# Kernel optimization log

Hardware: AMD Instinct MI355X
Metric: run time of the kernel (lower is better)

Reference implementation:

```python
import jax, jax.numpy as jnp
import numpy as np

B, L, S, H, E = 4, 1024, 1024, 16, 64
TOP_K = 10


def setup_inputs() -> dict:
    key = jax.random.key(0)
    kq, kk, kv = jax.random.split(key, 3)
    queries = jax.random.normal(kq, (B, L, H, E), dtype=jnp.float32)
    keys = jax.random.normal(kk, (B, S, H, E), dtype=jnp.float32)
    values = jax.random.normal(kv, (B, S, H, E), dtype=jnp.float32)
    return {"queries": queries, "keys": keys, "values": values}


def reference(queries, keys, values):
    Bq, Lq, Hq, Eq = queries.shape
    Sq = keys.shape[1]
    scale = 1.0 / np.sqrt(Eq).astype(np.float32)

    # FFT-based top-k frequency selection (mirrors torch: rfft over seq dim, ortho norm)
    keys_flat = keys.transpose(0, 2, 1, 3).reshape(Bq * Hq, Sq, Eq)  # [BH, S, E]
    freqs = jnp.fft.rfft(keys_flat, axis=1, norm='ortho')            # [BH, S//2+1, E]
    freq_mags = jnp.abs(freqs).mean(axis=-1)                          # [BH, S//2+1]
    k = min(TOP_K, Sq, freq_mags.shape[1])
    _, top_idx = jax.lax.top_k(freq_mags, k)                          # [BH, k]

    # Vectorized scatter of top-k indices into boolean position mask [BH, S]
    sparse_mask = jnp.zeros((Bq * Hq, Sq), dtype=bool)
    sparse_mask = sparse_mask.at[jnp.arange(Bq * Hq)[:, None], top_idx].set(True)
    sparse_mask = sparse_mask.reshape(Bq, Hq, Sq)                     # [B, H, S]

    # Dense masked attention
    scores = jnp.einsum('blhe,bshe->bhls', queries, keys) * scale     # [B, H, L, S]
    scores = jnp.where(sparse_mask[:, :, None, :], scores, -jnp.inf)
    attn = jax.nn.softmax(scores, axis=-1)                            # dropout: eval mode (identity)
    out = jnp.einsum('bhls,bshe->blhe', attn, values)                 # [B, L, H, E]
    return out, attn
```

## Files before the change

### kernel.cpp

```cpp
#include <hip/hip_runtime.h>
#include <math.h>

#define Bc 4
#define Lc 1024
#define Sc 1024
#define Hc 16
#define Ec 64
#define BHc 64
#define NF 513
#define TOPK 10
#define NCH 8
#define COLW 2304

#define PADW(w) ((w) + (((w) >> 4) << 1))
#define ZADDR(col, i) ((col) * COLW + PADW(2 * (i)))

__global__ __launch_bounds__(256) void zero_kernel(float4* __restrict__ dst,
                                                   int n4) {
  const int stride = gridDim.x * 256;
  for (int i = blockIdx.x * 256 + threadIdx.x; i < n4; i += stride)
    dst[i] = make_float4(0.f, 0.f, 0.f, 0.f);
}

__global__ __launch_bounds__(512) void fft4_kernel(
    const float* __restrict__ keys, float* __restrict__ pmag) {
  __shared__ float zbuf[4 * COLW];
  __shared__ float2 tw[1024];

  const int t   = threadIdx.x;
  const int blk = blockIdx.x;
  const int bh  = blk & 63;
  const int ch  = blk >> 6;
  const int b   = bh >> 4, h = bh & 15;

  for (int m = t; m < 1024; m += 512) {
    float sn, cs;
    sincosf(-6.28318530717958647692f * (float)m * (1.0f / 1024.0f), &sn, &cs);
    tw[m] = make_float2(cs, sn);
  }

  const float4* k4 = (const float4*)keys;
  const int fbase = b * 262144 + h * 16 + ch * 2;
  for (int i = t; i < 2048; i += 512) {
    const int s  = i >> 1;
    const int q4 = i & 1;
    float4 v = k4[fbase + s * 256 + q4];
    unsigned r = __brev((unsigned)s) >> 22;
    unsigned rs = ((r & 0x2AAu) >> 1) | ((r & 0x155u) << 1);
    *(float2*)&zbuf[ZADDR(2 * q4, rs)]     = make_float2(v.x, v.y);
    *(float2*)&zbuf[ZADDR(2 * q4 + 1, rs)] = make_float2(v.z, v.w);
  }
  __syncthreads();

  for (int st = 0; st < 5; ++st) {
    const int quarter = 1 << (2 * st);
    const int tstep   = 256 >> (2 * st);
#pragma unroll
    for (int rep = 0; rep < 2; ++rep) {
      const int task = t + rep * 512;
      const int col  = task >> 8;
      const int bf   = task & 255;
      const int j    = bf & (quarter - 1);
      const int bas  = ((bf >> (2 * st)) << (2 * st + 2)) + j;

      const float2 w1 = tw[j * tstep];
      const float2 w2 = tw[2 * j * tstep];
      const float2 w3 = tw[3 * j * tstep];

      float2 a  = *(const float2*)&zbuf[ZADDR(col, bas)];
      float2 bb = *(const float2*)&zbuf[ZADDR(col, bas + quarter)];
      float2 c  = *(const float2*)&zbuf[ZADDR(col, bas + 2 * quarter)];
      float2 d  = *(const float2*)&zbuf[ZADDR(col, bas + 3 * quarter)];

      float2 bw = make_float2(bb.x * w1.x - bb.y * w1.y, bb.x * w1.y + bb.y * w1.x);
      float2 cw = make_float2(c.x * w2.x - c.y * w2.y, c.x * w2.y + c.y * w2.x);
      float2 dw = make_float2(d.x * w3.x - d.y * w3.y, d.x * w3.y + d.y * w3.x);

      float2 s0 = make_float2(a.x + cw.x, a.y + cw.y);
      float2 s1 = make_float2(a.x - cw.x, a.y - cw.y);
      float2 s2 = make_float2(bw.x + dw.x, bw.y + dw.y);
      float2 s3 = make_float2(bw.x - dw.x, bw.y - dw.y);

      *(float2*)&zbuf[ZADDR(col, bas)]               = make_float2(s0.x + s2.x, s0.y + s2.y);
      *(float2*)&zbuf[ZADDR(col, bas + quarter)]     = make_float2(s1.x + s3.y, s1.y - s3.x);
      *(float2*)&zbuf[ZADDR(col, bas + 2 * quarter)] = make_float2(s0.x - s2.x, s0.y - s2.y);
      *(float2*)&zbuf[ZADDR(col, bas + 3 * quarter)] = make_float2(s1.x - s3.y, s1.y + s3.x);
    }
    __syncthreads();
  }

  for (int f = t; f < NF; f += 512) {
    const int nf = (1024 - f) & 1023;
    float ssum = 0.0f;
#pragma unroll
    for (int c = 0; c < 4; ++c) {
      float2 zf = *(const float2*)&zbuf[ZADDR(c, f)];
      float2 zn = *(const float2*)&zbuf[ZADDR(c, nf)];
      float xr = 0.5f * (zf.x + zn.x);
      float xi = 0.5f * (zf.y - zn.y);
      float yr = 0.5f * (zf.y + zn.y);
      float yi = 0.5f * (zn.x - zf.x);
      ssum += sqrtf(xr * xr + xi * xi) + sqrtf(yr * yr + yi * yi);
    }
    pmag[(size_t)blk * NF + f] = ssum;
  }
}

__global__ __launch_bounds__(64) void topk_kernel(
    const float* __restrict__ pmag, int* __restrict__ idx_out) {
  __shared__ float mag[NF];
  const int bh = blockIdx.x;
  const int t  = threadIdx.x;

  for (int f = t; f < NF; f += 64) {
    float s = 0.0f;
#pragma unroll
    for (int ch = 0; ch < NCH; ++ch)
      s += pmag[(size_t)(ch * 64 + bh) * NF + f];
    mag[f] = s;
  }
  __syncthreads();

  for (int r = 0; r < TOPK; ++r) {
    float bv = -INFINITY;
    int   bi = 0x7fffffff;
    for (int f = t; f < NF; f += 64) {
      float v = mag[f];
      if (v > bv || (v == bv && f < bi)) { bv = v; bi = f; }
    }
#pragma unroll
    for (int off = 32; off > 0; off >>= 1) {
      float ov = __shfl_xor(bv, off);
      int   oi = __shfl_xor(bi, off);
      if (ov > bv || (ov == bv && oi < bi)) { bv = ov; bi = oi; }
    }
    if (t == 0) {
      idx_out[bh * 16 + r] = bi;
      mag[bi] = -INFINITY;
    }
    __syncthreads();
  }
}

__global__ __launch_bounds__(256) void sparse_kernel(
    const float* __restrict__ qs, const float* __restrict__ ks,
    const float* __restrict__ vs, const int* __restrict__ idx,
    float* __restrict__ out, float* __restrict__ attn) {
  __shared__ float qt[64][65];
  __shared__ float kvt[2][TOPK][64];
  __shared__ float sc[64][13];
  __shared__ int   sid[TOPK];

  const int t    = threadIdx.x;
  const int bh   = blockIdx.x;
  const int b    = bh >> 4, h = bh & 15;
  const int l0   = blockIdx.y * 64;
  const int wave = t >> 6;
  const int lane = t & 63;

  if (t < TOPK) sid[t] = idx[bh * 16 + t];

  {
    const float4* q4 = (const float4*)qs;
    const int fb = b * 262144 + h * 16;
    for (int i = t; i < 1024; i += 256) {
      const int row = i >> 4, c4 = i & 15;
      float4 v = q4[fb + (l0 + row) * 256 + c4];
      qt[row][c4 * 4 + 0] = v.x;
      qt[row][c4 * 4 + 1] = v.y;
      qt[row][c4 * 4 + 2] = v.z;
      qt[row][c4 * 4 + 3] = v.w;
    }
  }
  __syncthreads();

  for (int i = t; i < 2 * TOPK * 64; i += 256) {
    const int kv = i >= TOPK * 64;
    const int j  = (i >> 6) - kv * TOPK;
    const int e  = i & 63;
    const float* src = kv ? vs : ks;
    kvt[kv][j][e] = src[(size_t)b * 1048576 + (size_t)sid[j] * 1024 + h * 64 + e];
  }
  __syncthreads();

#pragma unroll
  for (int r = 0; r < 3; ++r) {
    const int task = r * 256 + t;
    const int j = task >> 6;
    const int l = task & 63;
    if (j < TOPK) {
      float acc = 0.0f;
#pragma unroll 8
      for (int e = 0; e < 64; ++e) acc += qt[l][e] * kvt[0][j][e];
      sc[l][j] = acc * 0.125f;
    }
  }
  __syncthreads();

  if (t < 64) {
    float pv[TOPK];
    float mx = -INFINITY;
#pragma unroll
    for (int j = 0; j < TOPK; ++j) { pv[j] = sc[t][j]; mx = fmaxf(mx, pv[j]); }
    float sum = 0.0f;
#pragma unroll
    for (int j = 0; j < TOPK; ++j) { pv[j] = __expf(pv[j] - mx); sum += pv[j]; }
    float inv = 1.0f / sum;
#pragma unroll
    for (int j = 0; j < TOPK; ++j) sc[t][j] = pv[j] * inv;
  }
  __syncthreads();

  for (int li = 0; li < 16; ++li) {
    const int l = wave * 16 + li;

    float o = 0.0f;
#pragma unroll
    for (int j = 0; j < TOPK; ++j) o += sc[l][j] * kvt[1][j][lane];
    out[((size_t)b * 1024 + l0 + l) * 1024 + h * 64 + lane] = o;

    if (lane < TOPK)
      attn[((size_t)bh * 1024 + l0 + l) * 1024 + sid[lane]] = sc[l][lane];
  }
}

extern "C" void kernel_launch(void* const* d_in, const int* in_sizes, int n_in,
                              void* d_out, int out_size, void* d_ws,
                              size_t ws_size, hipStream_t stream) {
  (void)in_sizes; (void)n_in; (void)out_size; (void)ws_size;
  const float* qs = (const float*)d_in[0];
  const float* ks = (const float*)d_in[1];
  const float* vs = (const float*)d_in[2];

  float* out  = (float*)d_out;
  float* attn = out + (size_t)Bc * Lc * Hc * Ec;

  float* pmag = (float*)d_ws;
  int*   idxs = (int*)((char*)d_ws + (size_t)(NCH * BHc) * NF * sizeof(float));

  zero_kernel<<<2048, 256, 0, stream>>>((float4*)attn, 16777216);
  fft4_kernel<<<NCH * BHc, 512, 0, stream>>>(ks, pmag);
  topk_kernel<<<BHc, 64, 0, stream>>>(pmag, idxs);
  sparse_kernel<<<dim3(BHc, 16), 256, 0, stream>>>(qs, ks, vs, idxs, out, attn);
}
```

Baseline: 393.5 us.

## Fuse attn zero-fill into sparse kernel with full-row vectorized nontemporal stores

Removes the separate zero kernel that cleared the whole 256 MiB attention tensor and instead has the sparse kernel write every attention row in full: each lane precomputes which of its 16 columns match a top-k index and emits zeros or probabilities via 128-bit nontemporal stores. This avoids a second pass over attn (zero-fill then scattered writes) and one kernel launch. The output write is also made nontemporal, and the pmag layout is changed to bh-major. It adds per-element select logic and register use for the column map.

```diff
diff --git a/kernel.cpp b/kernel.cpp
--- a/kernel.cpp
+++ b/kernel.cpp
@@ -12,15 +12,10 @@
 #define NCH 8
 #define COLW 2304
 
+typedef float f32x4 __attribute__((ext_vector_type(4)));
+
 #define PADW(w) ((w) + (((w) >> 4) << 1))
 #define ZADDR(col, i) ((col) * COLW + PADW(2 * (i)))
-
-__global__ __launch_bounds__(256) void zero_kernel(float4* __restrict__ dst,
-                                                   int n4) {
-  const int stride = gridDim.x * 256;
-  for (int i = blockIdx.x * 256 + threadIdx.x; i < n4; i += stride)
-    dst[i] = make_float4(0.f, 0.f, 0.f, 0.f);
-}
 
 __global__ __launch_bounds__(512) void fft4_kernel(
     const float* __restrict__ keys, float* __restrict__ pmag) {
@@ -102,7 +97,7 @@
       float yi = 0.5f * (zn.x - zf.x);
       ssum += sqrtf(xr * xr + xi * xi) + sqrtf(yr * yr + yi * yi);
     }
-    pmag[(size_t)blk * NF + f] = ssum;
+    pmag[((size_t)bh * NCH + ch) * NF + f] = ssum;
   }
 }
 
@@ -116,7 +111,7 @@
     float s = 0.0f;
 #pragma unroll
     for (int ch = 0; ch < NCH; ++ch)
-      s += pmag[(size_t)(ch * 64 + bh) * NF + f];
+      s += pmag[((size_t)bh * NCH + ch) * NF + f];
     mag[f] = s;
   }
   __syncthreads();
@@ -174,6 +169,18 @@
   }
   __syncthreads();
 
+  int js[4][4];
+#pragma unroll
+  for (int i = 0; i < 4; ++i)
+#pragma unroll
+    for (int k = 0; k < 4; ++k) {
+      const int col = 4 * (lane + 64 * i) + k;
+      int sel = -1;
+#pragma unroll
+      for (int j = 0; j < TOPK; ++j) sel = (col == sid[j]) ? j : sel;
+      js[i][k] = sel;
+    }
+
   for (int i = t; i < 2 * TOPK * 64; i += 256) {
     const int kv = i >= TOPK * 64;
     const int j  = (i >> 6) - kv * TOPK;
@@ -214,13 +221,29 @@
   for (int li = 0; li < 16; ++li) {
     const int l = wave * 16 + li;
 
+    float p[TOPK];
+#pragma unroll
+    for (int j = 0; j < TOPK; ++j) p[j] = sc[l][j];
+
     float o = 0.0f;
 #pragma unroll
-    for (int j = 0; j < TOPK; ++j) o += sc[l][j] * kvt[1][j][lane];
-    out[((size_t)b * 1024 + l0 + l) * 1024 + h * 64 + lane] = o;
-
-    if (lane < TOPK)
-      attn[((size_t)bh * 1024 + l0 + l) * 1024 + sid[lane]] = sc[l][lane];
+    for (int j = 0; j < TOPK; ++j) o += p[j] * kvt[1][j][lane];
+    __builtin_nontemporal_store(
+        o, &out[((size_t)b * 1024 + l0 + l) * 1024 + h * 64 + lane]);
+
+    f32x4* arow = (f32x4*)(attn + ((size_t)bh * 1024 + l0 + l) * 1024);
+#pragma unroll
+    for (int i = 0; i < 4; ++i) {
+      f32x4 vv;
+#pragma unroll
+      for (int k = 0; k < 4; ++k) {
+        float x = 0.0f;
+#pragma unroll
+        for (int j = 0; j < TOPK; ++j) x = (js[i][k] == j) ? p[j] : x;
+        vv[k] = x;
+      }
+      __builtin_nontemporal_store(vv, &arow[lane + 64 * i]);
+    }
   }
 }
 
@@ -238,7 +261,6 @@
   float* pmag = (float*)d_ws;
   int*   idxs = (int*)((char*)d_ws + (size_t)(NCH * BHc) * NF * sizeof(float));
 
-  zero_kernel<<<2048, 256, 0, stream>>>((float4*)attn, 16777216);
   fft4_kernel<<<NCH * BHc, 512, 0, stream>>>(ks, pmag);
   topk_kernel<<<BHc, 64, 0, stream>>>(pmag, idxs);
   sparse_kernel<<<dim3(BHc, 16), 256, 0, stream>>>(qs, ks, vs, idxs, out, attn);
```

Result: faster. 372.0 us (-5.5%).
